# Optimization experiments

Measured on AMD Instinct MI355X. Metric: run time of the kernel, lower is better.

The kernel has to match this reference:

```python
import jax, jax.numpy as jnp
import numpy as np

# hardcoded constants from Model.sample_regions / gather_regions / __init__
RADIUS = 0.4
REGIONS = 50
BALL_K = 1000
TOP_K = 4
NEIGHBORHOOD = 128
COURSE = 512


def square_distance(src, dst):
    """src [B,N,C], dst [B,M,C] -> squared dists [B,N,M]."""
    d = -2.0 * jnp.einsum('bnc,bmc->bnm', src, dst)
    d = d + jnp.sum(src * src, -1)[:, :, None]
    d = d + jnp.sum(dst * dst, -1)[:, None, :]
    return d


def furthest_point_sample(xyz, npoint):
    """xyz [B,N,3] -> indices [B,npoint] (deterministic start at point 0)."""
    B, N, _ = xyz.shape
    barange = jnp.arange(B)

    def body(carry, _):
        dist, last = carry                      # dist [B,N], last [B] int32
        centroid = xyz[barange, last]           # [B,3]
        d = jnp.sum((xyz - centroid[:, None, :]) ** 2, -1)
        dist = jnp.minimum(dist, d)
        nxt = jnp.argmax(dist, axis=-1).astype(jnp.int32)
        return (dist, nxt), last

    init = (jnp.full((B, N), 1e10, xyz.dtype), jnp.zeros((B,), jnp.int32))
    _, idxs = jax.lax.scan(body, init, None, length=npoint)
    return jnp.transpose(idxs)                  # [B, npoint]


def knn_point(k, xyz, new_xyz):
    """k-NN of new_xyz [B,S,3] among xyz [B,N,3] -> idx [B,S,k]."""
    d = square_distance(new_xyz, xyz)
    _, idx = jax.lax.top_k(-d, k)
    return idx


def gather_xyz(xyz, idx):
    """xyz [B,N,3], idx [B,S] -> [B,S,3]."""
    B = xyz.shape[0]
    return xyz[jnp.arange(B)[:, None], idx]


def gather_regions(p_xyz, a_xyz, radius):
    """p_xyz [B,N,3] points, a_xyz [B,A,3] anchors -> [B, TOP_K*NEIGHBORHOOD, 3]."""
    B = p_xyz.shape[0]
    d2 = square_distance(a_xyz, p_xyz)                       # [B,A,N]
    counts = jnp.minimum(jnp.sum(d2 < radius * radius, axis=2), BALL_K)
    _, topk_idx = jax.lax.top_k(counts, TOP_K)               # densest anchors [B,TOP_K]
    sel = gather_xyz(a_xyz, topk_idx)                        # [B,TOP_K,3]
    nidx = knn_point(NEIGHBORHOOD, p_xyz, sel)               # [B,TOP_K,NB]
    neigh = p_xyz[jnp.arange(B)[:, None, None], nidx]        # [B,TOP_K,NB,3]
    return neigh.reshape(B, TOP_K * NEIGHBORHOOD, 3)


def sample_regions(p_xyz, regions, r):
    anchors_idx = furthest_point_sample(p_xyz, regions)
    anchors = gather_xyz(p_xyz, anchors_idx)
    return gather_regions(p_xyz, anchors, r)


def setup_inputs() -> dict:
    key = jax.random.key(0)
    points = jax.random.normal(key, (16, 3, 16384), dtype=jnp.float32)
    return {"points": points}


def reference(points):
    # points [B,3,N] -> p_xyz [B,N,3]
    p_xyz = jnp.transpose(points, (0, 2, 1))
    roi1 = sample_regions(p_xyz, REGIONS, RADIUS)            # [B,512,3]
    roi2 = sample_regions(p_xyz, REGIONS, RADIUS)            # [B,512,3] (a == b == 0.4)
    fps_idx = furthest_point_sample(p_xyz, COURSE)           # [B,512]
    fps_pts = gather_xyz(p_xyz, fps_idx)                     # [B,512,3]
    return jnp.concatenate([roi1, roi2, fps_pts], axis=1)    # [B,1536,3]
```

## Files before the change

kernel.cpp:

```cpp
#include <hip/hip_runtime.h>
#include <stdint.h>

#define NPTS 16384
#define BATCH 16
#define FPS_N 512
#define NANCH 50
#define TOPK 4
#define NBH 128
#define BALLK 1000

#define FT 1024
#define FPAIRS 8

#define FPS_SMEM (65536 + 65536 + 2 * 16 * 8)

#define CTRL_XOR1 0xB1
#define CTRL_XOR2 0x4E
#define CTRL_ROR4 0x124
#define CTRL_ROR8 0x128

#define DPP_MAX64(v, CTRL) do {                                                   \
  unsigned int _lo = (unsigned int)(v);                                           \
  unsigned int _hi = (unsigned int)((v) >> 32);                                   \
  unsigned int _slo = (unsigned int)__builtin_amdgcn_update_dpp((int)_lo, (int)_lo, CTRL, 0xf, 0xf, false); \
  unsigned int _shi = (unsigned int)__builtin_amdgcn_update_dpp((int)_hi, (int)_hi, CTRL, 0xf, 0xf, false); \
  unsigned long long _o = (((unsigned long long)_shi) << 32) | _slo;              \
  if (_o > (v)) (v) = _o;                                                         \
} while (0)

#define DPP_MIN64(v, CTRL) do {                                                   \
  unsigned int _lo = (unsigned int)(v);                                           \
  unsigned int _hi = (unsigned int)((v) >> 32);                                   \
  unsigned int _slo = (unsigned int)__builtin_amdgcn_update_dpp((int)_lo, (int)_lo, CTRL, 0xf, 0xf, false); \
  unsigned int _shi = (unsigned int)__builtin_amdgcn_update_dpp((int)_hi, (int)_hi, CTRL, 0xf, 0xf, false); \
  unsigned long long _o = (((unsigned long long)_shi) << 32) | _slo;              \
  if (_o < (v)) (v) = _o;                                                         \
} while (0)

#define SWZ16_MIN64(v) do {                                                       \
  unsigned int _lo = (unsigned int)(v), _hi = (unsigned int)((v) >> 32);          \
  unsigned int _slo = (unsigned int)__builtin_amdgcn_ds_swizzle((int)_lo, 0x401f);\
  unsigned int _shi = (unsigned int)__builtin_amdgcn_ds_swizzle((int)_hi, 0x401f);\
  unsigned long long _o = (((unsigned long long)_shi) << 32) | _slo;              \
  if (_o < (v)) (v) = _o;                                                         \
} while (0)

#define SHF32_MIN64(v) do {                                                       \
  unsigned long long _o = __shfl_xor((v), 32, 64);                                \
  if (_o < (v)) (v) = _o;                                                         \
} while (0)

__global__ __launch_bounds__(FT, 4) void fps_kernel(const float* __restrict__ pts,
                                                    int* __restrict__ fps_idx) {
  extern __shared__ char smem[];
  float2* __restrict__ X2 = (float2*)smem;
  float2* __restrict__ Y2 = (float2*)(smem + 65536);
  unsigned long long* __restrict__ waveres =
      (unsigned long long*)(smem + 131072);

  const int b = blockIdx.x;
  const int t = threadIdx.x;
  const float* __restrict__ px = pts + (size_t)b * 3 * NPTS;
  const float* __restrict__ py = px + NPTS;
  const float* __restrict__ pz = py + NPTS;

  float2 z2[FPAIRS], dist2[FPAIRS];
#pragma unroll
  for (int j = 0; j < FPAIRS; ++j) {
    const int i2 = (j << 11) + (t << 1);
    X2[(j << 10) + t] = *(const float2*)&px[i2];
    Y2[(j << 10) + t] = *(const float2*)&py[i2];
    z2[j] = *(const float2*)&pz[i2];
    dist2[j] = make_float2(1e10f, 1e10f);
  }
  if (t == 0) fps_idx[b * FPS_N] = 0;
  float bx = px[0], by = py[0], bz = pz[0];
  const int wS = __builtin_amdgcn_readfirstlane(t >> 6);
  __syncthreads();

  for (int step = 1; step < FPS_N; ++step) {
    const float nbx = -bx, nby = -by, nbz = -bz;
    const float2 nbx2 = make_float2(nbx, nbx);
    const float2 nby2 = make_float2(nby, nby);
    const float2 nbz2 = make_float2(nbz, nbz);
    float run = -1.0f;
#pragma unroll
    for (int j = 0; j < FPAIRS; ++j) {
      const float2 Xp = X2[(j << 10) + t];
      const float2 Yp = Y2[(j << 10) + t];
      float2 t0, t1, t2;
      asm("v_pk_add_f32 %0, %3, %6\n\t"
          "v_pk_add_f32 %1, %4, %7\n\t"
          "v_pk_add_f32 %2, %5, %8\n\t"
          "v_pk_mul_f32 %0, %0, %0\n\t"
          "v_pk_mul_f32 %1, %1, %1\n\t"
          "v_pk_mul_f32 %2, %2, %2\n\t"
          "v_pk_add_f32 %0, %0, %1\n\t"
          "v_pk_add_f32 %0, %0, %2"
          : "=&v"(t0), "=&v"(t1), "=&v"(t2)
          : "v"(Xp), "v"(Yp), "v"(z2[j]), "v"(nbx2), "v"(nby2), "v"(nbz2));
      dist2[j].x = fminf(dist2[j].x, t0.x);
      dist2[j].y = fminf(dist2[j].y, t0.y);
      asm("v_max3_f32 %0, %0, %1, %2"
          : "+v"(run) : "v"(dist2[j].x), "v"(dist2[j].y));
    }
    uint32_t m = __float_as_uint(run);
    {
      uint32_t s;
      s = (uint32_t)__builtin_amdgcn_update_dpp((int)m, (int)m, CTRL_XOR1, 0xf, 0xf, false); m = m > s ? m : s;
      s = (uint32_t)__builtin_amdgcn_update_dpp((int)m, (int)m, CTRL_XOR2, 0xf, 0xf, false); m = m > s ? m : s;
      s = (uint32_t)__builtin_amdgcn_update_dpp((int)m, (int)m, CTRL_ROR4, 0xf, 0xf, false); m = m > s ? m : s;
      s = (uint32_t)__builtin_amdgcn_update_dpp((int)m, (int)m, CTRL_ROR8, 0xf, 0xf, false); m = m > s ? m : s;
      s = (uint32_t)__builtin_amdgcn_ds_swizzle((int)m, 0x401f);                              m = m > s ? m : s;
      s = (uint32_t)__shfl_xor((int)m, 32, 64);                                              m = m > s ? m : s;
    }
    const float gmaxf = __uint_as_float(m);
    uint32_t widx_w = 0xFFFFFFFFu;
#pragma unroll
    for (int j = 0; j < FPAIRS; ++j) {
      const unsigned long long b0 = __ballot(dist2[j].x == gmaxf);
      const unsigned long long b1 = __ballot(dist2[j].y == gmaxf);
      const unsigned long long cb = b0 | b1;
      if (cb) {
        const int l = (int)__builtin_ctzll(cb);
        const uint32_t p = ((b0 >> l) & 1ull) ? 0u : 1u;
        const uint32_t cand = ((uint32_t)j << 11) + ((uint32_t)((wS << 6) | l) << 1) + p;
        widx_w = widx_w < cand ? widx_w : cand;
      }
    }
    const unsigned long long key =
        ((unsigned long long)m << 32) | (uint32_t)(~widx_w);
    const int par = step & 1;
    if ((t & 63) == 0) waveres[par * 16 + wS] = key;
    __syncthreads();
    unsigned long long g = waveres[par * 16 + (t & 15)];
    DPP_MAX64(g, CTRL_XOR1);
    DPP_MAX64(g, CTRL_XOR2);
    DPP_MAX64(g, CTRL_ROR4);
    DPP_MAX64(g, CTRL_ROR8);
    const uint32_t widx = ~(uint32_t)g;
    if (t == 0) fps_idx[b * FPS_N + step] = (int)widx;
    const int si = __builtin_amdgcn_readfirstlane((int)widx);
    bx = px[si]; by = py[si]; bz = pz[si];
  }
}

__global__ __launch_bounds__(256) void count_kernel(const float* __restrict__ pts,
                                                    const int* __restrict__ fps_idx,
                                                    int* __restrict__ counts) {
  const int b = blockIdx.y, a = blockIdx.x;
  const int tid = threadIdx.x;
  const float* __restrict__ px = pts + (size_t)b * 3 * NPTS;
  const float* __restrict__ py = px + NPTS;
  const float* __restrict__ pz = py + NPTS;
  const int aidx = fps_idx[b * FPS_N + a];
  const float ax = px[aidx], ay = py[aidx], az = pz[aidx];
  const float asum = __fadd_rn(__fadd_rn(__fmul_rn(ax, ax), __fmul_rn(ay, ay)),
                               __fmul_rn(az, az));
  const float R2 = (float)(0.4 * 0.4);
  int cnt = 0;
  for (int i = tid; i < NPTS; i += 256) {
    const float X = px[i], Y = py[i], Z = pz[i];
    const float dot = __fadd_rn(__fadd_rn(__fmul_rn(ax, X), __fmul_rn(ay, Y)),
                                __fmul_rn(az, Z));
    const float psum = __fadd_rn(__fadd_rn(__fmul_rn(X, X), __fmul_rn(Y, Y)),
                                 __fmul_rn(Z, Z));
    const float d = __fadd_rn(__fadd_rn(__fmul_rn(-2.0f, dot), asum), psum);
    cnt += (d < R2) ? 1 : 0;
  }
#pragma unroll
  for (int off = 32; off > 0; off >>= 1) cnt += __shfl_xor(cnt, off, 64);
  __shared__ int ws[4];
  if ((tid & 63) == 0) ws[tid >> 6] = cnt;
  __syncthreads();
  if (tid == 0) {
    int c = ws[0] + ws[1] + ws[2] + ws[3];
    counts[b * NANCH + a] = c < BALLK ? c : BALLK;
  }
}

__global__ void top4_kernel(const int* __restrict__ counts,
                            const int* __restrict__ fps_idx,
                            int* __restrict__ top4pt) {
  const int b = threadIdx.x;
  if (b >= BATCH) return;
  unsigned long long used = 0ULL;
  for (int r = 0; r < TOPK; ++r) {
    int bestc = -1, besta = 0;
    for (int a = 0; a < NANCH; ++a) {
      if (used & (1ULL << a)) continue;
      const int c = counts[b * NANCH + a];
      if (c > bestc) { bestc = c; besta = a; }
    }
    used |= 1ULL << besta;
    top4pt[b * TOPK + r] = fps_idx[b * FPS_N + besta];
  }
}

#define KT 1024
#define KPPT (NPTS / KT)

__device__ __forceinline__ uint32_t f2key(float f) {
  uint32_t u = __float_as_uint(f);
  return (u & 0x80000000u) ? ~u : (u | 0x80000000u);
}

__global__ __launch_bounds__(KT) void knn_kernel(const float* __restrict__ pts,
                                                 const int* __restrict__ top4pt,
                                                 int* __restrict__ nn_idx) {
  const int b = blockIdx.y, j = blockIdx.x;
  const int tid = threadIdx.x;
  const float* __restrict__ px = pts + (size_t)b * 3 * NPTS;
  const float* __restrict__ py = px + NPTS;
  const float* __restrict__ pz = py + NPTS;
  const int aidx = top4pt[b * TOPK + j];
  const float ax = px[aidx], ay = py[aidx], az = pz[aidx];
  const float asum = __fadd_rn(__fadd_rn(__fmul_rn(ax, ax), __fmul_rn(ay, ay)),
                               __fmul_rn(az, az));
  unsigned long long key[KPPT];
#pragma unroll
  for (int k = 0; k < KPPT; ++k) {
    const int i = tid + k * KT;
    const float X = px[i], Y = py[i], Z = pz[i];
    const float dot = __fadd_rn(__fadd_rn(__fmul_rn(ax, X), __fmul_rn(ay, Y)),
                                __fmul_rn(az, Z));
    const float psum = __fadd_rn(__fadd_rn(__fmul_rn(X, X), __fmul_rn(Y, Y)),
                                 __fmul_rn(Z, Z));
    const float d = __fadd_rn(__fadd_rn(__fmul_rn(-2.0f, dot), asum), psum);
    key[k] = ((unsigned long long)f2key(d) << 32) | (uint32_t)i;
  }
  __shared__ unsigned long long waveres[2][16];
  for (int t = 0; t < NBH; ++t) {
    unsigned long long m01 = key[0] < key[1] ? key[0] : key[1];
    unsigned long long m23 = key[2] < key[3] ? key[2] : key[3];
    unsigned long long m45 = key[4] < key[5] ? key[4] : key[5];
    unsigned long long m67 = key[6] < key[7] ? key[6] : key[7];
    unsigned long long m89 = key[8] < key[9] ? key[8] : key[9];
    unsigned long long mab = key[10] < key[11] ? key[10] : key[11];
    unsigned long long mcd = key[12] < key[13] ? key[12] : key[13];
    unsigned long long mef = key[14] < key[15] ? key[14] : key[15];
    unsigned long long m0 = m01 < m23 ? m01 : m23;
    unsigned long long m1 = m45 < m67 ? m45 : m67;
    unsigned long long m2 = m89 < mab ? m89 : mab;
    unsigned long long m3 = mcd < mef ? mcd : mef;
    unsigned long long ma = m0 < m1 ? m0 : m1;
    unsigned long long mb = m2 < m3 ? m2 : m3;
    unsigned long long m = ma < mb ? ma : mb;

    DPP_MIN64(m, CTRL_XOR1);
    DPP_MIN64(m, CTRL_XOR2);
    DPP_MIN64(m, CTRL_ROR4);
    DPP_MIN64(m, CTRL_ROR8);
    SWZ16_MIN64(m);
    SHF32_MIN64(m);

    const int par = t & 1;
    if ((tid & 63) == 0) waveres[par][tid >> 6] = m;
    __syncthreads();
    unsigned long long g = waveres[par][tid & 15];
    DPP_MIN64(g, CTRL_XOR1);
    DPP_MIN64(g, CTRL_XOR2);
    DPP_MIN64(g, CTRL_ROR4);
    DPP_MIN64(g, CTRL_ROR8);

    if (tid == 0) nn_idx[(b * TOPK + j) * NBH + t] = (int)(uint32_t)g;
#pragma unroll
    for (int k = 0; k < KPPT; ++k)
      if (key[k] == g) key[k] = ~0ULL;
  }
}

__global__ __launch_bounds__(512) void gather_kernel(const float* __restrict__ pts,
                                                     const int* __restrict__ nn_idx,
                                                     const int* __restrict__ fps_idx,
                                                     float* __restrict__ out) {
  const int b = blockIdx.x, t = threadIdx.x;
  const float* __restrict__ px = pts + (size_t)b * 3 * NPTS;
  const float* __restrict__ py = px + NPTS;
  const float* __restrict__ pz = py + NPTS;
  for (int s = t; s < 1536; s += 512) {
    int src;
    if (s < 1024) src = nn_idx[b * 512 + (s & 511)];
    else          src = fps_idx[b * FPS_N + (s - 1024)];
    float* o = out + ((size_t)b * 1536 + s) * 3;
    o[0] = px[src]; o[1] = py[src]; o[2] = pz[src];
  }
}

extern "C" void kernel_launch(void* const* d_in, const int* in_sizes, int n_in,
                              void* d_out, int out_size, void* d_ws, size_t ws_size,
                              hipStream_t stream) {
  const float* pts = (const float*)d_in[0];
  float* out = (float*)d_out;
  char* ws = (char*)d_ws;
  int* fps_idx = (int*)(ws);
  int* counts  = (int*)(ws + 32768);
  int* top4pt  = (int*)(ws + 40960);
  int* nn_idx  = (int*)(ws + 49152);

  hipFuncSetAttribute((const void*)fps_kernel,
                      hipFuncAttributeMaxDynamicSharedMemorySize, FPS_SMEM);

  fps_kernel<<<dim3(BATCH), dim3(FT), FPS_SMEM, stream>>>(pts, fps_idx);
  count_kernel<<<dim3(NANCH, BATCH), dim3(256), 0, stream>>>(pts, fps_idx, counts);
  top4_kernel<<<dim3(1), dim3(64), 0, stream>>>(counts, fps_idx, top4pt);
  knn_kernel<<<dim3(TOPK, BATCH), dim3(KT), 0, stream>>>(pts, top4pt, nn_idx);
  gather_kernel<<<dim3(BATCH), dim3(512), 0, stream>>>(pts, nn_idx, fps_idx, out);
}
```

Before: 1.073 ms.

## Fuse FPS, ball count, top-4 and kNN into one concurrent mega kernel

Replaces the five-kernel pipeline with a single launch of 80 blocks. Sixteen blocks run the 512-step FPS. Sixty-four blocks each redo a short 50-step FPS, then count points within the radius of each anchor, pick the top-4 anchors, and run kNN from shared-memory coordinates, all without global round trips. This removes launch gaps and lets the region work overlap the long FPS, at the cost of repeating the 50-step FPS four times per batch element. Blocks shrink to 512 threads with 16 point pairs per thread, which raises register pressure and halves the threads per FPS block.

```diff
diff --git a/kernel.cpp b/kernel.cpp
--- a/kernel.cpp
+++ b/kernel.cpp
@@ -9,10 +9,17 @@
 #define NBH 128
 #define BALLK 1000
 
-#define FT 1024
-#define FPAIRS 8
-
-#define FPS_SMEM (65536 + 65536 + 2 * 16 * 8)
+#define FT 512
+#define PAIRS 16
+
+#define OFF_X2 0
+#define OFF_Y2 65536
+#define OFF_FPSIDX 131072
+#define OFF_CNT    (OFF_FPSIDX + 2048)
+#define OFF_WRED   (OFF_CNT + 256)
+#define OFF_T4     (OFF_WRED + 128)
+#define OFF_KNN    (OFF_T4 + 16)
+#define SMEM_TOTAL (OFF_KNN + 512)
 
 #define CTRL_XOR1 0xB1
 #define CTRL_XOR2 0x4E
@@ -50,44 +57,57 @@
   if (_o < (v)) (v) = _o;                                                         \
 } while (0)
 
-__global__ __launch_bounds__(FT, 4) void fps_kernel(const float* __restrict__ pts,
-                                                    int* __restrict__ fps_idx) {
+__device__ __forceinline__ uint32_t f2key(float f) {
+  uint32_t u = __float_as_uint(f);
+  return (u & 0x80000000u) ? ~u : (u | 0x80000000u);
+}
+
+__global__ __launch_bounds__(FT, 2) void mega_kernel(const float* __restrict__ pts,
+                                                     float* __restrict__ out) {
   extern __shared__ char smem[];
-  float2* __restrict__ X2 = (float2*)smem;
-  float2* __restrict__ Y2 = (float2*)(smem + 65536);
-  unsigned long long* __restrict__ waveres =
-      (unsigned long long*)(smem + 131072);
-
-  const int b = blockIdx.x;
+  float2* __restrict__ X2 = (float2*)(smem + OFF_X2);
+  float2* __restrict__ Y2 = (float2*)(smem + OFF_Y2);
+  int* __restrict__ fpsidx = (int*)(smem + OFF_FPSIDX);
+  int* __restrict__ cnt = (int*)(smem + OFF_CNT);
+  unsigned long long* __restrict__ wred = (unsigned long long*)(smem + OFF_WRED);
+  int* __restrict__ t4 = (int*)(smem + OFF_T4);
+  int* __restrict__ knnidx = (int*)(smem + OFF_KNN);
+
+  const int bid = blockIdx.x;
+  const bool isFps = bid < BATCH;
+  const int b = isFps ? bid : ((bid - BATCH) >> 2);
+  const int j = isFps ? 0 : ((bid - BATCH) & 3);
+  const int nsteps = isFps ? FPS_N : NANCH;
+
   const int t = threadIdx.x;
+  const int wS = __builtin_amdgcn_readfirstlane(t >> 6);
   const float* __restrict__ px = pts + (size_t)b * 3 * NPTS;
   const float* __restrict__ py = px + NPTS;
   const float* __restrict__ pz = py + NPTS;
 
-  float2 z2[FPAIRS], dist2[FPAIRS];
-#pragma unroll
-  for (int j = 0; j < FPAIRS; ++j) {
-    const int i2 = (j << 11) + (t << 1);
-    X2[(j << 10) + t] = *(const float2*)&px[i2];
-    Y2[(j << 10) + t] = *(const float2*)&py[i2];
-    z2[j] = *(const float2*)&pz[i2];
-    dist2[j] = make_float2(1e10f, 1e10f);
-  }
-  if (t == 0) fps_idx[b * FPS_N] = 0;
+  float2 z2[PAIRS], dist2[PAIRS];
+#pragma unroll
+  for (int k = 0; k < PAIRS; ++k) {
+    const int i2 = (k << 10) + (t << 1);
+    X2[(k << 9) + t] = *(const float2*)&px[i2];
+    Y2[(k << 9) + t] = *(const float2*)&py[i2];
+    z2[k] = *(const float2*)&pz[i2];
+    dist2[k] = make_float2(1e10f, 1e10f);
+  }
+  if (t == 0) fpsidx[0] = 0;
   float bx = px[0], by = py[0], bz = pz[0];
-  const int wS = __builtin_amdgcn_readfirstlane(t >> 6);
-  __syncthreads();
-
-  for (int step = 1; step < FPS_N; ++step) {
+  __syncthreads();
+
+  for (int step = 1; step < nsteps; ++step) {
     const float nbx = -bx, nby = -by, nbz = -bz;
     const float2 nbx2 = make_float2(nbx, nbx);
     const float2 nby2 = make_float2(nby, nby);
     const float2 nbz2 = make_float2(nbz, nbz);
     float run = -1.0f;
 #pragma unroll
-    for (int j = 0; j < FPAIRS; ++j) {
-      const float2 Xp = X2[(j << 10) + t];
-      const float2 Yp = Y2[(j << 10) + t];
+    for (int k = 0; k < PAIRS; ++k) {
+      const float2 Xp = X2[(k << 9) + t];
+      const float2 Yp = Y2[(k << 9) + t];
       float2 t0, t1, t2;
       asm("v_pk_add_f32 %0, %3, %6\n\t"
           "v_pk_add_f32 %1, %4, %7\n\t"
@@ -98,11 +118,11 @@
           "v_pk_add_f32 %0, %0, %1\n\t"
           "v_pk_add_f32 %0, %0, %2"
           : "=&v"(t0), "=&v"(t1), "=&v"(t2)
-          : "v"(Xp), "v"(Yp), "v"(z2[j]), "v"(nbx2), "v"(nby2), "v"(nbz2));
-      dist2[j].x = fminf(dist2[j].x, t0.x);
-      dist2[j].y = fminf(dist2[j].y, t0.y);
+          : "v"(Xp), "v"(Yp), "v"(z2[k]), "v"(nbx2), "v"(nby2), "v"(nbz2));
+      dist2[k].x = fminf(dist2[k].x, t0.x);
+      dist2[k].y = fminf(dist2[k].y, t0.y);
       asm("v_max3_f32 %0, %0, %1, %2"
-          : "+v"(run) : "v"(dist2[j].x), "v"(dist2[j].y));
+          : "+v"(run) : "v"(dist2[k].x), "v"(dist2[k].y));
     }
     uint32_t m = __float_as_uint(run);
     {
@@ -117,135 +137,134 @@
     const float gmaxf = __uint_as_float(m);
     uint32_t widx_w = 0xFFFFFFFFu;
 #pragma unroll
-    for (int j = 0; j < FPAIRS; ++j) {
-      const unsigned long long b0 = __ballot(dist2[j].x == gmaxf);
-      const unsigned long long b1 = __ballot(dist2[j].y == gmaxf);
+    for (int k = 0; k < PAIRS; ++k) {
+      const unsigned long long b0 = __ballot(dist2[k].x == gmaxf);
+      const unsigned long long b1 = __ballot(dist2[k].y == gmaxf);
       const unsigned long long cb = b0 | b1;
       if (cb) {
         const int l = (int)__builtin_ctzll(cb);
         const uint32_t p = ((b0 >> l) & 1ull) ? 0u : 1u;
-        const uint32_t cand = ((uint32_t)j << 11) + ((uint32_t)((wS << 6) | l) << 1) + p;
+        const uint32_t cand = ((uint32_t)k << 10) + ((uint32_t)((wS << 6) | l) << 1) + p;
         widx_w = widx_w < cand ? widx_w : cand;
       }
     }
     const unsigned long long key =
         ((unsigned long long)m << 32) | (uint32_t)(~widx_w);
     const int par = step & 1;
-    if ((t & 63) == 0) waveres[par * 16 + wS] = key;
+    if ((t & 63) == 0) wred[par * 8 + wS] = key;
     __syncthreads();
-    unsigned long long g = waveres[par * 16 + (t & 15)];
+    unsigned long long g = wred[par * 8 + (t & 7)];
     DPP_MAX64(g, CTRL_XOR1);
     DPP_MAX64(g, CTRL_XOR2);
     DPP_MAX64(g, CTRL_ROR4);
-    DPP_MAX64(g, CTRL_ROR8);
     const uint32_t widx = ~(uint32_t)g;
-    if (t == 0) fps_idx[b * FPS_N + step] = (int)widx;
+    if (t == 0) fpsidx[step] = (int)widx;
     const int si = __builtin_amdgcn_readfirstlane((int)widx);
     bx = px[si]; by = py[si]; bz = pz[si];
   }
-}
-
-__global__ __launch_bounds__(256) void count_kernel(const float* __restrict__ pts,
-                                                    const int* __restrict__ fps_idx,
-                                                    int* __restrict__ counts) {
-  const int b = blockIdx.y, a = blockIdx.x;
-  const int tid = threadIdx.x;
-  const float* __restrict__ px = pts + (size_t)b * 3 * NPTS;
-  const float* __restrict__ py = px + NPTS;
-  const float* __restrict__ pz = py + NPTS;
-  const int aidx = fps_idx[b * FPS_N + a];
-  const float ax = px[aidx], ay = py[aidx], az = pz[aidx];
+
+  if (isFps) {
+    __syncthreads();
+    const int idx = fpsidx[t];
+    const float X = px[idx], Y = py[idx], Z = pz[idx];
+    float* o = out + ((size_t)b * 1536 + 1024 + t) * 3;
+    o[0] = X; o[1] = Y; o[2] = Z;
+    return;
+  }
+
+  const float R2 = (float)(0.4 * 0.4);
+
+  if (t < 64) cnt[t] = 0;
+  __syncthreads();
+  for (int a = 0; a < NANCH; ++a) {
+    const int ai = fpsidx[a];
+    const float ax = px[ai], ay = py[ai], az = pz[ai];
+    const float asum = __fadd_rn(__fadd_rn(__fmul_rn(ax, ax), __fmul_rn(ay, ay)),
+                                 __fmul_rn(az, az));
+    int local = 0;
+#pragma unroll
+    for (int k = 0; k < PAIRS; ++k) {
+      const float2 Xp = X2[(k << 9) + t];
+      const float2 Yp = Y2[(k << 9) + t];
+      const float2 Zp = z2[k];
+      {
+        const float dot = __fadd_rn(__fadd_rn(__fmul_rn(ax, Xp.x), __fmul_rn(ay, Yp.x)),
+                                    __fmul_rn(az, Zp.x));
+        const float ps = __fadd_rn(__fadd_rn(__fmul_rn(Xp.x, Xp.x), __fmul_rn(Yp.x, Yp.x)),
+                                   __fmul_rn(Zp.x, Zp.x));
+        const float d = __fadd_rn(__fadd_rn(__fmul_rn(-2.0f, dot), asum), ps);
+        local += (d < R2) ? 1 : 0;
+      }
+      {
+        const float dot = __fadd_rn(__fadd_rn(__fmul_rn(ax, Xp.y), __fmul_rn(ay, Yp.y)),
+                                    __fmul_rn(az, Zp.y));
+        const float ps = __fadd_rn(__fadd_rn(__fmul_rn(Xp.y, Xp.y), __fmul_rn(Yp.y, Yp.y)),
+                                   __fmul_rn(Zp.y, Zp.y));
+        const float d = __fadd_rn(__fadd_rn(__fmul_rn(-2.0f, dot), asum), ps);
+        local += (d < R2) ? 1 : 0;
+      }
+    }
+#pragma unroll
+    for (int off = 32; off > 0; off >>= 1) local += __shfl_xor(local, off, 64);
+    if ((t & 63) == 0) atomicAdd(&cnt[a], local);
+  }
+  __syncthreads();
+
+  if (t == 0) {
+    unsigned long long used = 0ULL;
+    for (int r = 0; r < TOPK; ++r) {
+      int bestc = -1, besta = 0;
+      for (int a = 0; a < NANCH; ++a) {
+        if (used & (1ULL << a)) continue;
+        int c = cnt[a];
+        c = c < BALLK ? c : BALLK;
+        if (c > bestc) { bestc = c; besta = a; }
+      }
+      used |= 1ULL << besta;
+      t4[r] = fpsidx[besta];
+    }
+  }
+  __syncthreads();
+
+  const int ai = t4[j];
+  const float ax = px[ai], ay = py[ai], az = pz[ai];
   const float asum = __fadd_rn(__fadd_rn(__fmul_rn(ax, ax), __fmul_rn(ay, ay)),
                                __fmul_rn(az, az));
-  const float R2 = (float)(0.4 * 0.4);
-  int cnt = 0;
-  for (int i = tid; i < NPTS; i += 256) {
-    const float X = px[i], Y = py[i], Z = pz[i];
-    const float dot = __fadd_rn(__fadd_rn(__fmul_rn(ax, X), __fmul_rn(ay, Y)),
-                                __fmul_rn(az, Z));
-    const float psum = __fadd_rn(__fadd_rn(__fmul_rn(X, X), __fmul_rn(Y, Y)),
-                                 __fmul_rn(Z, Z));
-    const float d = __fadd_rn(__fadd_rn(__fmul_rn(-2.0f, dot), asum), psum);
-    cnt += (d < R2) ? 1 : 0;
-  }
-#pragma unroll
-  for (int off = 32; off > 0; off >>= 1) cnt += __shfl_xor(cnt, off, 64);
-  __shared__ int ws[4];
-  if ((tid & 63) == 0) ws[tid >> 6] = cnt;
-  __syncthreads();
-  if (tid == 0) {
-    int c = ws[0] + ws[1] + ws[2] + ws[3];
-    counts[b * NANCH + a] = c < BALLK ? c : BALLK;
-  }
-}
-
-__global__ void top4_kernel(const int* __restrict__ counts,
-                            const int* __restrict__ fps_idx,
-                            int* __restrict__ top4pt) {
-  const int b = threadIdx.x;
-  if (b >= BATCH) return;
-  unsigned long long used = 0ULL;
-  for (int r = 0; r < TOPK; ++r) {
-    int bestc = -1, besta = 0;
-    for (int a = 0; a < NANCH; ++a) {
-      if (used & (1ULL << a)) continue;
-      const int c = counts[b * NANCH + a];
-      if (c > bestc) { bestc = c; besta = a; }
-    }
-    used |= 1ULL << besta;
-    top4pt[b * TOPK + r] = fps_idx[b * FPS_N + besta];
-  }
-}
-
-#define KT 1024
-#define KPPT (NPTS / KT)
-
-__device__ __forceinline__ uint32_t f2key(float f) {
-  uint32_t u = __float_as_uint(f);
-  return (u & 0x80000000u) ? ~u : (u | 0x80000000u);
-}
-
-__global__ __launch_bounds__(KT) void knn_kernel(const float* __restrict__ pts,
-                                                 const int* __restrict__ top4pt,
-                                                 int* __restrict__ nn_idx) {
-  const int b = blockIdx.y, j = blockIdx.x;
-  const int tid = threadIdx.x;
-  const float* __restrict__ px = pts + (size_t)b * 3 * NPTS;
-  const float* __restrict__ py = px + NPTS;
-  const float* __restrict__ pz = py + NPTS;
-  const int aidx = top4pt[b * TOPK + j];
-  const float ax = px[aidx], ay = py[aidx], az = pz[aidx];
-  const float asum = __fadd_rn(__fadd_rn(__fmul_rn(ax, ax), __fmul_rn(ay, ay)),
-                               __fmul_rn(az, az));
-  unsigned long long key[KPPT];
-#pragma unroll
-  for (int k = 0; k < KPPT; ++k) {
-    const int i = tid + k * KT;
-    const float X = px[i], Y = py[i], Z = pz[i];
-    const float dot = __fadd_rn(__fadd_rn(__fmul_rn(ax, X), __fmul_rn(ay, Y)),
-                                __fmul_rn(az, Z));
-    const float psum = __fadd_rn(__fadd_rn(__fmul_rn(X, X), __fmul_rn(Y, Y)),
-                                 __fmul_rn(Z, Z));
-    const float d = __fadd_rn(__fadd_rn(__fmul_rn(-2.0f, dot), asum), psum);
-    key[k] = ((unsigned long long)f2key(d) << 32) | (uint32_t)i;
-  }
-  __shared__ unsigned long long waveres[2][16];
-  for (int t = 0; t < NBH; ++t) {
-    unsigned long long m01 = key[0] < key[1] ? key[0] : key[1];
-    unsigned long long m23 = key[2] < key[3] ? key[2] : key[3];
-    unsigned long long m45 = key[4] < key[5] ? key[4] : key[5];
-    unsigned long long m67 = key[6] < key[7] ? key[6] : key[7];
-    unsigned long long m89 = key[8] < key[9] ? key[8] : key[9];
-    unsigned long long mab = key[10] < key[11] ? key[10] : key[11];
-    unsigned long long mcd = key[12] < key[13] ? key[12] : key[13];
-    unsigned long long mef = key[14] < key[15] ? key[14] : key[15];
-    unsigned long long m0 = m01 < m23 ? m01 : m23;
-    unsigned long long m1 = m45 < m67 ? m45 : m67;
-    unsigned long long m2 = m89 < mab ? m89 : mab;
-    unsigned long long m3 = mcd < mef ? mcd : mef;
-    unsigned long long ma = m0 < m1 ? m0 : m1;
-    unsigned long long mb = m2 < m3 ? m2 : m3;
-    unsigned long long m = ma < mb ? ma : mb;
+  unsigned long long kk[2 * PAIRS];
+#pragma unroll
+  for (int k = 0; k < PAIRS; ++k) {
+    const int i2 = (k << 10) + (t << 1);
+    const float2 Xp = X2[(k << 9) + t];
+    const float2 Yp = Y2[(k << 9) + t];
+    const float2 Zp = z2[k];
+    {
+      const float dot = __fadd_rn(__fadd_rn(__fmul_rn(ax, Xp.x), __fmul_rn(ay, Yp.x)),
+                                  __fmul_rn(az, Zp.x));
+      const float ps = __fadd_rn(__fadd_rn(__fmul_rn(Xp.x, Xp.x), __fmul_rn(Yp.x, Yp.x)),
+                                 __fmul_rn(Zp.x, Zp.x));
+      const float d = __fadd_rn(__fadd_rn(__fmul_rn(-2.0f, dot), asum), ps);
+      kk[2 * k] = ((unsigned long long)f2key(d) << 32) | (uint32_t)i2;
+    }
+    {
+      const float dot = __fadd_rn(__fadd_rn(__fmul_rn(ax, Xp.y), __fmul_rn(ay, Yp.y)),
+                                  __fmul_rn(az, Zp.y));
+      const float ps = __fadd_rn(__fadd_rn(__fmul_rn(Xp.y, Xp.y), __fmul_rn(Yp.y, Yp.y)),
+                                 __fmul_rn(Zp.y, Zp.y));
+      const float d = __fadd_rn(__fadd_rn(__fmul_rn(-2.0f, dot), asum), ps);
+      kk[2 * k + 1] = ((unsigned long long)f2key(d) << 32) | (uint32_t)(i2 + 1);
+    }
+  }
+  for (int r = 0; r < NBH; ++r) {
+    unsigned long long v16[16];
+#pragma unroll
+    for (int k = 0; k < 16; ++k) v16[k] = kk[2 * k] < kk[2 * k + 1] ? kk[2 * k] : kk[2 * k + 1];
+#pragma unroll
+    for (int k = 0; k < 8; ++k) v16[k] = v16[k] < v16[k + 8] ? v16[k] : v16[k + 8];
+#pragma unroll
+    for (int k = 0; k < 4; ++k) v16[k] = v16[k] < v16[k + 4] ? v16[k] : v16[k + 4];
+    unsigned long long m0 = v16[0] < v16[2] ? v16[0] : v16[2];
+    unsigned long long m1 = v16[1] < v16[3] ? v16[1] : v16[3];
+    unsigned long long m = m0 < m1 ? m0 : m1;
 
     DPP_MIN64(m, CTRL_XOR1);
     DPP_MIN64(m, CTRL_XOR2);
@@ -254,36 +273,27 @@
     SWZ16_MIN64(m);
     SHF32_MIN64(m);
 
-    const int par = t & 1;
-    if ((tid & 63) == 0) waveres[par][tid >> 6] = m;
+    const int par = r & 1;
+    if ((t & 63) == 0) wred[par * 8 + wS] = m;
     __syncthreads();
-    unsigned long long g = waveres[par][tid & 15];
+    unsigned long long g = wred[par * 8 + (t & 7)];
     DPP_MIN64(g, CTRL_XOR1);
     DPP_MIN64(g, CTRL_XOR2);
     DPP_MIN64(g, CTRL_ROR4);
-    DPP_MIN64(g, CTRL_ROR8);
-
-    if (tid == 0) nn_idx[(b * TOPK + j) * NBH + t] = (int)(uint32_t)g;
-#pragma unroll
-    for (int k = 0; k < KPPT; ++k)
-      if (key[k] == g) key[k] = ~0ULL;
-  }
-}
-
-__global__ __launch_bounds__(512) void gather_kernel(const float* __restrict__ pts,
-                                                     const int* __restrict__ nn_idx,
-                                                     const int* __restrict__ fps_idx,
-                                                     float* __restrict__ out) {
-  const int b = blockIdx.x, t = threadIdx.x;
-  const float* __restrict__ px = pts + (size_t)b * 3 * NPTS;
-  const float* __restrict__ py = px + NPTS;
-  const float* __restrict__ pz = py + NPTS;
-  for (int s = t; s < 1536; s += 512) {
-    int src;
-    if (s < 1024) src = nn_idx[b * 512 + (s & 511)];
-    else          src = fps_idx[b * FPS_N + (s - 1024)];
-    float* o = out + ((size_t)b * 1536 + s) * 3;
-    o[0] = px[src]; o[1] = py[src]; o[2] = pz[src];
+    if (t == 0) knnidx[r] = (int)(uint32_t)g;
+#pragma unroll
+    for (int k = 0; k < 2 * PAIRS; ++k)
+      if (kk[k] == g) kk[k] = ~0ULL;
+  }
+  __syncthreads();
+
+  if (t < NBH) {
+    const int idx = knnidx[t];
+    const float X = px[idx], Y = py[idx], Z = pz[idx];
+    float* o1 = out + ((size_t)b * 1536 + (j << 7) + t) * 3;
+    float* o2 = o1 + 512 * 3;
+    o1[0] = X; o1[1] = Y; o1[2] = Z;
+    o2[0] = X; o2[1] = Y; o2[2] = Z;
   }
 }
 
@@ -292,18 +302,9 @@
                               hipStream_t stream) {
   const float* pts = (const float*)d_in[0];
   float* out = (float*)d_out;
-  char* ws = (char*)d_ws;
-  int* fps_idx = (int*)(ws);
-  int* counts  = (int*)(ws + 32768);
-  int* top4pt  = (int*)(ws + 40960);
-  int* nn_idx  = (int*)(ws + 49152);
-
-  hipFuncSetAttribute((const void*)fps_kernel,
-                      hipFuncAttributeMaxDynamicSharedMemorySize, FPS_SMEM);
-
-  fps_kernel<<<dim3(BATCH), dim3(FT), FPS_SMEM, stream>>>(pts, fps_idx);
-  count_kernel<<<dim3(NANCH, BATCH), dim3(256), 0, stream>>>(pts, fps_idx, counts);
-  top4_kernel<<<dim3(1), dim3(64), 0, stream>>>(counts, fps_idx, top4pt);
-  knn_kernel<<<dim3(TOPK, BATCH), dim3(KT), 0, stream>>>(pts, top4pt, nn_idx);
-  gather_kernel<<<dim3(BATCH), dim3(512), 0, stream>>>(pts, nn_idx, fps_idx, out);
+  (void)d_ws; (void)ws_size;
+
+  hipFuncSetAttribute((const void*)mega_kernel,
+                      hipFuncAttributeMaxDynamicSharedMemorySize, SMEM_TOTAL);
+  mega_kernel<<<dim3(BATCH + BATCH * TOPK), dim3(FT), SMEM_TOTAL, stream>>>(pts, out);
 }
```

Result: faster. 987.2 us (-8.0%).
